# Optimization experiments

Measured on AMD Instinct MI355X. Metric: run time of the kernel, lower is better.

The kernel has to match this reference:

```python
import jax, jax.numpy as jnp
import numpy as np

NUM_CLASSES = 3
LAMBDA_COORD = 5.0
B, A, N = 1048576, 3, 8  # batch, anchors (hardcoded 3 in source), gt boxes per image


def setup_inputs() -> dict:
    key = jax.random.key(0)
    k1, k2, k3 = jax.random.split(key, 3)
    predictions = jax.random.normal(k1, (B, A, 5 + NUM_CLASSES), dtype=jnp.float32)
    gt_boxes = jax.random.uniform(k2, (B, N, 4), dtype=jnp.float32)  # x,y,w,h
    gt_classes = jax.random.randint(k3, (B, N), 0, NUM_CLASSES, dtype=jnp.int32)
    return {"predictions": predictions, "gt_boxes": gt_boxes, "gt_classes": gt_classes}


def reference(predictions, gt_boxes, gt_classes):
    batch = predictions.shape[0]
    # decode predictions, shapes (B, A)
    px = jax.nn.sigmoid(predictions[..., 0])
    py = jax.nn.sigmoid(predictions[..., 1])
    pw = predictions[..., 2]
    ph = predictions[..., 3]
    pconf = jax.nn.sigmoid(predictions[..., 4])
    plogits = predictions[..., 5:]  # (B, A, C)

    # pred corners (B, A, 1)
    px1 = (px - pw / 2)[..., None]; px2 = (px + pw / 2)[..., None]
    py1 = (py - ph / 2)[..., None]; py2 = (py + ph / 2)[..., None]
    # gt corners (B, 1, N)
    gx = gt_boxes[..., 0][:, None, :]; gy = gt_boxes[..., 1][:, None, :]
    gw = gt_boxes[..., 2][:, None, :]; gh = gt_boxes[..., 3][:, None, :]
    gx1 = gx - gw / 2; gx2 = gx + gw / 2
    gy1 = gy - gh / 2; gy2 = gy + gh / 2

    inter_w = jnp.clip(jnp.minimum(px2, gx2) - jnp.maximum(px1, gx1), 0.0)
    inter_h = jnp.clip(jnp.minimum(py2, gy2) - jnp.maximum(py1, gy1), 0.0)
    inter = inter_w * inter_h                              # (B, A, N)
    pred_area = (px2 - px1) * (py2 - py1)                  # (B, A, 1)
    gt_area = (gx2 - gx1) * (gy2 - gy1)                    # (B, 1, N)
    iou = inter / (pred_area + gt_area - inter + 1e-6)     # (B, A, N)

    best_iou = jnp.max(iou, axis=-1)                       # (B, A)
    best_idx = jnp.argmax(iou, axis=-1)                    # (B, A) -- first max, matches strict-> loop
    matched = best_iou > 0.5                               # (B, A)

    mb = jnp.take_along_axis(gt_boxes, best_idx[:, :, None], axis=1)   # (B, A, 4)
    mcls = jnp.take_along_axis(gt_classes, best_idx, axis=1)           # (B, A)

    # coordinate loss: per-scalar mse on matched anchors
    coord = (px - mb[..., 0]) ** 2 + (py - mb[..., 1]) ** 2 \
          + (pw - mb[..., 2]) ** 2 + (ph - mb[..., 3]) ** 2
    coord_loss = jnp.sum(jnp.where(matched, coord, 0.0))

    # confidence BCE, target 1 if matched else 0 (torch BCE clamps log at -100)
    logp = jnp.maximum(jnp.log(pconf), -100.0)
    log1mp = jnp.maximum(jnp.log1p(-pconf), -100.0)
    conf_loss = jnp.sum(jnp.where(matched, -logp, -log1mp))

    # class cross-entropy on matched anchors
    logsm = jax.nn.log_softmax(plogits, axis=-1)                        # (B, A, C)
    nll = -jnp.take_along_axis(logsm, mcls[..., None], axis=-1)[..., 0]  # (B, A)
    class_loss = jnp.sum(jnp.where(matched, nll, 0.0))

    total = LAMBDA_COORD * coord_loss + conf_loss + class_loss
    return total / batch
```

## Files before the change

kernel.cpp:

```cpp
#include <hip/hip_runtime.h>

#define B_SIZE 1048576
#define NBLK   4096

__device__ __forceinline__ float frcp(float x) { return __builtin_amdgcn_rcpf(x); }

__global__ __launch_bounds__(256) void yolo_loss_kernel(
    const float* __restrict__ pred,
    const float* __restrict__ gt_boxes,
    const int*   __restrict__ gt_classes,
    double* __restrict__ part) {
    __shared__ float sP[4][64 * 25];
    __shared__ float sG[4][64 * 33];
    __shared__ float sRed[4];

    const int tid  = threadIdx.x;
    const int wave = tid >> 6;
    const int lane = tid & 63;
    const int wb   = blockIdx.x * 256 + wave * 64;

    const float4* pA = reinterpret_cast<const float4*>(pred     + (size_t)wb * 24);
    const float4* gA = reinterpret_cast<const float4*>(gt_boxes + (size_t)wb * 32);
    float4 vp[6], vg[8];
    #pragma unroll
    for (int k = 0; k < 6; ++k) vp[k] = pA[k * 64 + lane];
    #pragma unroll
    for (int k = 0; k < 8; ++k) vg[k] = gA[k * 64 + lane];
    const int4* cme = reinterpret_cast<const int4*>(gt_classes + (size_t)(wb + lane) * 8);
    const int4 c0 = cme[0], c1 = cme[1];

    float* sp = sP[wave];
    float* sg = sG[wave];
    #pragma unroll
    for (int k = 0; k < 6; ++k) {
        const unsigned f = k * 64 + lane;
        const unsigned bl = f / 6u, of = f % 6u;
        float* d = &sp[bl * 25 + of * 4];
        d[0] = vp[k].x; d[1] = vp[k].y; d[2] = vp[k].z; d[3] = vp[k].w;
    }
    #pragma unroll
    for (int k = 0; k < 8; ++k) {
        const unsigned f = k * 64 + lane;
        const unsigned bl = f >> 3, of = f & 7;
        float* d = &sg[bl * 33 + of * 4];
        d[0] = vg[k].x; d[1] = vg[k].y; d[2] = vg[k].z; d[3] = vg[k].w;
    }
    float pr[24];
    #pragma unroll
    for (int w = 0; w < 24; ++w) pr[w] = sp[lane * 25 + w];
    float gb[32];
    #pragma unroll
    for (int w = 0; w < 32; ++w) gb[w] = sg[lane * 33 + w];
    const int gc[8] = {c0.x, c0.y, c0.z, c0.w, c1.x, c1.y, c1.z, c1.w};

    float total = 0.0f;
    #pragma unroll
    for (int a = 0; a < 3; ++a) {
        const float* p = pr + a * 8;
        const float px = frcp(1.0f + __expf(-p[0]));
        const float py = frcp(1.0f + __expf(-p[1]));
        const float pw = p[2];
        const float ph = p[3];
        const float z  = p[4];
        const float px1 = px - pw * 0.5f, px2 = px + pw * 0.5f;
        const float py1 = py - ph * 0.5f, py2 = py + ph * 0.5f;
        const float pa_eps = (px2 - px1) * (py2 - py1) + 1e-6f;

        float best_iou = -3.4e38f;
        int best_idx = 0;
        #pragma unroll
        for (int n = 0; n < 8; ++n) {
            const float gx = gb[n*4+0], gy = gb[n*4+1];
            const float gw = gb[n*4+2], gh = gb[n*4+3];
            const float hw = gw * 0.5f, hh = gh * 0.5f;
            const float iw = fmaxf(fminf(px2, gx + hw) - fmaxf(px1, gx - hw), 0.0f);
            const float ih = fmaxf(fminf(py2, gy + hh) - fmaxf(py1, gy - hh), 0.0f);
            const float inter = iw * ih;
            const float iou = inter * frcp((pa_eps + gw * gh) - inter);
            const bool upd = iou > best_iou;
            best_iou = upd ? iou : best_iou;
            best_idx = upd ? n : best_idx;
        }
        const bool matched = best_iou > 0.5f;

        float mbx = gb[0], mby = gb[1], mbw = gb[2], mbh = gb[3];
        int mcls = gc[0];
        #pragma unroll
        for (int n = 1; n < 8; ++n) {
            const bool s = (best_idx == n);
            mbx = s ? gb[n*4+0] : mbx;
            mby = s ? gb[n*4+1] : mby;
            mbw = s ? gb[n*4+2] : mbw;
            mbh = s ? gb[n*4+3] : mbh;
            mcls = s ? gc[n] : mcls;
        }

        const float az = fabsf(z);
        const float c  = __logf(1.0f + __expf(-az));
        const float sp_pos = fmaxf(z, 0.0f) + c;
        const float sp_neg = fmaxf(-z, 0.0f) + c;
        total += fminf(matched ? sp_neg : sp_pos, 100.0f);

        if (matched) {
            const float dx = px - mbx, dy = py - mby;
            const float dw = pw - mbw, dh = ph - mbh;
            total += 5.0f * (dx*dx + dy*dy + dw*dw + dh*dh);
            const float l0 = p[5], l1 = p[6], l2 = p[7];
            const float m = fmaxf(l0, fmaxf(l1, l2));
            const float lse = m + __logf(__expf(l0-m) + __expf(l1-m) + __expf(l2-m));
            const float sel = (mcls == 0) ? l0 : ((mcls == 1) ? l1 : l2);
            total += lse - sel;
        }
    }

    #pragma unroll
    for (int off = 32; off > 0; off >>= 1)
        total += __shfl_down(total, off, 64);
    if (lane == 0) sRed[wave] = total;
    __syncthreads();
    if (tid == 0) {
        part[blockIdx.x] = (double)sRed[0] + (double)sRed[1]
                         + (double)sRed[2] + (double)sRed[3];
    }
}

__global__ __launch_bounds__(256) void yolo_reduce_kernel(
    const double* __restrict__ part, float* __restrict__ out) {
    double s = 0.0;
    #pragma unroll
    for (int k = 0; k < NBLK / 256; ++k)
        s += part[threadIdx.x + k * 256];
    #pragma unroll
    for (int off = 32; off > 0; off >>= 1)
        s += __shfl_down(s, off, 64);
    __shared__ double r[4];
    const int lane = threadIdx.x & 63;
    const int wave = threadIdx.x >> 6;
    if (lane == 0) r[wave] = s;
    __syncthreads();
    if (threadIdx.x == 0)
        out[0] = (float)((r[0] + r[1] + r[2] + r[3]) / (double)B_SIZE);
}

extern "C" void kernel_launch(void* const* d_in, const int* in_sizes, int n_in,
                              void* d_out, int out_size, void* d_ws, size_t ws_size,
                              hipStream_t stream) {
    const float* pred       = (const float*)d_in[0];
    const float* gt_boxes   = (const float*)d_in[1];
    const int*   gt_classes = (const int*)d_in[2];
    float* out   = (float*)d_out;
    double* part = (double*)d_ws;

    yolo_loss_kernel<<<NBLK, 256, 0, stream>>>(pred, gt_boxes, gt_classes, part);
    yolo_reduce_kernel<<<1, 256, 0, stream>>>(part, out);
}
```

Before: 274.0 us.

## Drop LDS transpose staging in favour of direct per-thread vector loads

Removes the shared-memory staging, in which each wave loaded predictions and boxes with coalesced float4 reads and then transposed them through padded LDS. Each thread now reads its own 96-byte prediction row, 128-byte box row and class row directly with float4 loads. Block size grows from 256 to 1024 threads, which gives fewer blocks and a 16-way final block reduction. This cuts the LDS traffic and the index arithmetic. The cost is that each load instruction across a wave now hits addresses strided by 96 or 128 bytes, so memory coalescing depends on L1/L2 catching the reuse between instructions.

Result: slower. 284.6 us (+3.9%).

```diff
diff --git a/kernel.cpp b/kernel.cpp
--- a/kernel.cpp
+++ b/kernel.cpp
@@ -1,57 +1,33 @@
 #include <hip/hip_runtime.h>
 
 #define B_SIZE 1048576
-#define NBLK   4096
+#define TPB    1024
+#define NBLK   (B_SIZE / TPB)
 
 __device__ __forceinline__ float frcp(float x) { return __builtin_amdgcn_rcpf(x); }
 
-__global__ __launch_bounds__(256) void yolo_loss_kernel(
+__global__ __launch_bounds__(TPB) void yolo_loss_kernel(
     const float* __restrict__ pred,
     const float* __restrict__ gt_boxes,
     const int*   __restrict__ gt_classes,
     double* __restrict__ part) {
-    __shared__ float sP[4][64 * 25];
-    __shared__ float sG[4][64 * 33];
-    __shared__ float sRed[4];
+    const int tid = threadIdx.x;
+    const int b   = blockIdx.x * TPB + tid;
 
-    const int tid  = threadIdx.x;
-    const int wave = tid >> 6;
-    const int lane = tid & 63;
-    const int wb   = blockIdx.x * 256 + wave * 64;
+    float pr[24];
+    const float4* pv4 = reinterpret_cast<const float4*>(pred + (size_t)b * 24);
+    #pragma unroll
+    for (int i = 0; i < 6; ++i) reinterpret_cast<float4*>(pr)[i] = pv4[i];
 
-    const float4* pA = reinterpret_cast<const float4*>(pred     + (size_t)wb * 24);
-    const float4* gA = reinterpret_cast<const float4*>(gt_boxes + (size_t)wb * 32);
-    float4 vp[6], vg[8];
+    float gb[32];
+    const float4* gv4 = reinterpret_cast<const float4*>(gt_boxes + (size_t)b * 32);
     #pragma unroll
-    for (int k = 0; k < 6; ++k) vp[k] = pA[k * 64 + lane];
+    for (int i = 0; i < 8; ++i) reinterpret_cast<float4*>(gb)[i] = gv4[i];
+
+    int gc[8];
+    const int4* gc4 = reinterpret_cast<const int4*>(gt_classes + (size_t)b * 8);
     #pragma unroll
-    for (int k = 0; k < 8; ++k) vg[k] = gA[k * 64 + lane];
-    const int4* cme = reinterpret_cast<const int4*>(gt_classes + (size_t)(wb + lane) * 8);
-    const int4 c0 = cme[0], c1 = cme[1];
-
-    float* sp = sP[wave];
-    float* sg = sG[wave];
-    #pragma unroll
-    for (int k = 0; k < 6; ++k) {
-        const unsigned f = k * 64 + lane;
-        const unsigned bl = f / 6u, of = f % 6u;
-        float* d = &sp[bl * 25 + of * 4];
-        d[0] = vp[k].x; d[1] = vp[k].y; d[2] = vp[k].z; d[3] = vp[k].w;
-    }
-    #pragma unroll
-    for (int k = 0; k < 8; ++k) {
-        const unsigned f = k * 64 + lane;
-        const unsigned bl = f >> 3, of = f & 7;
-        float* d = &sg[bl * 33 + of * 4];
-        d[0] = vg[k].x; d[1] = vg[k].y; d[2] = vg[k].z; d[3] = vg[k].w;
-    }
-    float pr[24];
-    #pragma unroll
-    for (int w = 0; w < 24; ++w) pr[w] = sp[lane * 25 + w];
-    float gb[32];
-    #pragma unroll
-    for (int w = 0; w < 32; ++w) gb[w] = sg[lane * 33 + w];
-    const int gc[8] = {c0.x, c0.y, c0.z, c0.w, c1.x, c1.y, c1.z, c1.w};
+    for (int i = 0; i < 2; ++i) reinterpret_cast<int4*>(gc)[i] = gc4[i];
 
     float total = 0.0f;
     #pragma unroll
@@ -116,11 +92,16 @@
     #pragma unroll
     for (int off = 32; off > 0; off >>= 1)
         total += __shfl_down(total, off, 64);
-    if (lane == 0) sRed[wave] = total;
+    __shared__ float smem[16];
+    const int lane = tid & 63;
+    const int wid  = tid >> 6;
+    if (lane == 0) smem[wid] = total;
     __syncthreads();
     if (tid == 0) {
-        part[blockIdx.x] = (double)sRed[0] + (double)sRed[1]
-                         + (double)sRed[2] + (double)sRed[3];
+        double s = 0.0;
+        #pragma unroll
+        for (int w = 0; w < 16; ++w) s += (double)smem[w];
+        part[blockIdx.x] = s;
     }
 }
 
@@ -151,6 +132,6 @@
     float* out   = (float*)d_out;
     double* part = (double*)d_ws;
 
-    yolo_loss_kernel<<<NBLK, 256, 0, stream>>>(pred, gt_boxes, gt_classes, part);
+    yolo_loss_kernel<<<NBLK, TPB, 0, stream>>>(pred, gt_boxes, gt_classes, part);
     yolo_reduce_kernel<<<1, 256, 0, stream>>>(part, out);
 }
```
